# Performance work log

Measured on AMD Instinct MI355X. Metric: run time of the kernel, lower is better.

## Reference

```python
import jax, jax.numpy as jnp
import numpy as np

N, K, D = 2_000_000, 16, 3
EPS = 1e-6  # matches torch eye*1e-6 jitter added to the diagonal covariance


def setup_inputs() -> dict:
    key = jax.random.key(0)
    k1, k2, k3, k4 = jax.random.split(key, 4)
    x = jax.random.normal(k1, (N, D), dtype=jnp.float32)
    means = jax.random.normal(k2, (K, D), dtype=jnp.float32)
    # positive diagonal variances
    covariances = jax.random.uniform(k3, (K, D), dtype=jnp.float32, minval=0.5, maxval=2.0)
    w = jax.random.uniform(k4, (K,), dtype=jnp.float32, minval=0.1, maxval=1.0)
    weights = w / jnp.sum(w)  # mixture weights sum to 1
    return {"x": x, "means": means, "covariances": covariances, "weights": weights}


def reference(x, means, covariances, weights):
    # scale_tril of diag(cov)+eps*I is diag(sqrt(cov+eps))
    scale = jnp.sqrt(covariances + EPS)                      # [K, D]
    # standardized residuals: [N, K, D]
    z = (x[:, None, :] - means[None, :, :]) / scale[None, :, :]
    log_det = jnp.sum(jnp.log(scale), axis=-1)               # [K], log|L|
    d = x.shape[-1]
    # per-component Gaussian log-prob + log mixture weight: [N, K]
    log_prob = (-0.5 * (d * jnp.log(2.0 * jnp.pi) + jnp.sum(z * z, axis=-1))
                - log_det[None, :] + jnp.log(weights)[None, :])
    # mixture log-likelihood per point: [N]
    return jax.nn.logsumexp(log_prob, axis=1)
```

## Files before the change

### kernel.cpp

```cpp
#include <hip/hip_runtime.h>


constexpr int KCOMP = 16;
constexpr float EPS = 1e-6f;
#define LOG2E 1.4426950408889634f
#define LN2   0.6931471805599453f

__global__ __launch_bounds__(256) void gmm_loglik_kernel(
    const float* __restrict__ x,
    const float* __restrict__ means,
    const float* __restrict__ cov,
    const float* __restrict__ weights,
    float* __restrict__ out,
    int ngrp)
{
    __shared__ float4 s_cf[KCOMP * 2];

    const int t = threadIdx.x;
    if (t < KCOMP) {
        float v0 = cov[3 * t + 0] + EPS;
        float v1 = cov[3 * t + 1] + EPS;
        float v2 = cov[3 * t + 2] + EPS;
        float m0 = means[3 * t + 0];
        float m1 = means[3 * t + 1];
        float m2 = means[3 * t + 2];
        float h0 = 0.5f / v0, h1 = 0.5f / v1, h2 = 0.5f / v2;
        float ck = -2.7568155996140185f
                 - 0.5f * (__logf(v0) + __logf(v1) + __logf(v2))
                 + __logf(weights[t]);
        float A = ck - (h0 * m0 * m0 + h1 * m1 * m1 + h2 * m2 * m2);
        s_cf[2 * t + 0] = make_float4(LOG2E * A,
                                      LOG2E * 2.f * h0 * m0,
                                      LOG2E * 2.f * h1 * m1,
                                      LOG2E * 2.f * h2 * m2);
        s_cf[2 * t + 1] = make_float4(-LOG2E * h0, -LOG2E * h1, -LOG2E * h2, 0.f);
    }
    __syncthreads();

    const int g = blockIdx.x * blockDim.x + t;
    if (g >= ngrp) return;

    const float4* __restrict__ x4 = (const float4*)x;
    float4 a = x4[3 * g + 0];
    float4 b = x4[3 * g + 1];
    float4 c = x4[3 * g + 2];

    float px[4] = {a.x, a.w, b.z, c.y};
    float py[4] = {a.y, b.x, b.w, c.z};
    float pz[4] = {a.z, b.y, c.x, c.w};
    float res[4];

#pragma unroll
    for (int p = 0; p < 4; ++p) {
        const float X = px[p], Y = py[p], Z = pz[p];
        const float X2 = X * X, Y2 = Y * Y, Z2 = Z * Z;
        float lp[KCOMP];
        float mx = -3.4e38f;
#pragma unroll
        for (int k = 0; k < KCOMP; ++k) {
            float4 u = s_cf[2 * k + 0];
            float4 v = s_cf[2 * k + 1];
            float q = fmaf(u.y, X, u.x);
            q = fmaf(u.z, Y, q);
            q = fmaf(u.w, Z, q);
            q = fmaf(v.x, X2, q);
            q = fmaf(v.y, Y2, q);
            q = fmaf(v.z, Z2, q);
            lp[k] = q;
            mx = fmaxf(mx, q);
        }
        float s = 0.f;
#pragma unroll
        for (int k = 0; k < KCOMP; ++k)
            s += exp2f(lp[k] - mx);
        res[p] = LN2 * (mx + log2f(s));
    }

    ((float4*)out)[g] = make_float4(res[0], res[1], res[2], res[3]);
}

__global__ void gmm_tail_kernel(
    const float* __restrict__ x,
    const float* __restrict__ means,
    const float* __restrict__ cov,
    const float* __restrict__ weights,
    float* __restrict__ out,
    int start, int n)
{
    int i = start + blockIdx.x * blockDim.x + threadIdx.x;
    if (i >= n) return;
    float X = x[3 * i], Y = x[3 * i + 1], Z = x[3 * i + 2];
    float lp[KCOMP];
    float mx = -3.4e38f;
#pragma unroll
    for (int k = 0; k < KCOMP; ++k) {
        float v0 = cov[3 * k] + EPS, v1 = cov[3 * k + 1] + EPS, v2 = cov[3 * k + 2] + EPS;
        float dx = X - means[3 * k], dy = Y - means[3 * k + 1], dz = Z - means[3 * k + 2];
        float q = -2.7568155996140185f
                - 0.5f * (__logf(v0) + __logf(v1) + __logf(v2))
                + __logf(weights[k])
                - 0.5f * (dx * dx / v0 + dy * dy / v1 + dz * dz / v2);
        lp[k] = q;
        mx = fmaxf(mx, q);
    }
    float s = 0.f;
#pragma unroll
    for (int k = 0; k < KCOMP; ++k)
        s += __expf(lp[k] - mx);
    out[i] = mx + __logf(s);
}

extern "C" void kernel_launch(void* const* d_in, const int* in_sizes, int n_in,
                              void* d_out, int out_size, void* d_ws, size_t ws_size,
                              hipStream_t stream) {
    const float* x       = (const float*)d_in[0];
    const float* means   = (const float*)d_in[1];
    const float* cov     = (const float*)d_in[2];
    const float* weights = (const float*)d_in[3];
    float* out           = (float*)d_out;

    const int n = in_sizes[0] / 3;
    const int ngrp = n >> 2;
    if (ngrp > 0) {
        int blocks = (ngrp + 255) / 256;
        gmm_loglik_kernel<<<blocks, 256, 0, stream>>>(x, means, cov, weights, out, ngrp);
    }
    const int rem = n - (ngrp << 2);
    if (rem > 0) {
        gmm_tail_kernel<<<1, 64, 0, stream>>>(x, means, cov, weights, out, ngrp << 2, n);
    }
}
```

Measured before the change: 84.49 us.

## Stage points through LDS with coalesced loads and use packed FP32 FMA

Loads each block's point data cooperatively into shared memory with coalesced float4 reads, so per-thread strided 48-byte loads become contiguous ones. Processes the four points per thread as two 2-wide vectors so the compiler can emit packed FP32 FMA/max instructions, and swaps exp2f/log2f for the raw amdgcn intrinsics. This trades extra LDS traffic and a barrier for fewer VALU instructions. The kernel was compute-bound on the quadratic form and exp evaluations.

New measurement: 82.45 us. -2.4%, faster.

```diff
diff --git a/kernel.cpp b/kernel.cpp
--- a/kernel.cpp
+++ b/kernel.cpp
@@ -6,15 +6,20 @@
 #define LOG2E 1.4426950408889634f
 #define LN2   0.6931471805599453f
 
+typedef float v2f __attribute__((ext_vector_type(2)));
+static __device__ __forceinline__ v2f sp(float s) { return (v2f){s, s}; }
+
 __global__ __launch_bounds__(256) void gmm_loglik_kernel(
     const float* __restrict__ x,
     const float* __restrict__ means,
     const float* __restrict__ cov,
     const float* __restrict__ weights,
     float* __restrict__ out,
-    int ngrp)
+    int nmain)
 {
-    __shared__ float4 s_cf[KCOMP * 2];
+    __shared__ float4 s_pts4[768];
+    __shared__ float4 s_u[KCOMP];
+    __shared__ float4 s_v[KCOMP];
 
     const int t = threadIdx.x;
     if (t < KCOMP) {
@@ -29,54 +34,76 @@
                  - 0.5f * (__logf(v0) + __logf(v1) + __logf(v2))
                  + __logf(weights[t]);
         float A = ck - (h0 * m0 * m0 + h1 * m1 * m1 + h2 * m2 * m2);
-        s_cf[2 * t + 0] = make_float4(LOG2E * A,
-                                      LOG2E * 2.f * h0 * m0,
-                                      LOG2E * 2.f * h1 * m1,
-                                      LOG2E * 2.f * h2 * m2);
-        s_cf[2 * t + 1] = make_float4(-LOG2E * h0, -LOG2E * h1, -LOG2E * h2, 0.f);
+        s_u[t] = make_float4(LOG2E * A,
+                             LOG2E * 2.f * h0 * m0,
+                             LOG2E * 2.f * h1 * m1,
+                             LOG2E * 2.f * h2 * m2);
+        s_v[t] = make_float4(-LOG2E * h0, -LOG2E * h1, -LOG2E * h2, 0.f);
+    }
+
+    const float4* __restrict__ x4 = (const float4*)x;
+    const int n4 = (nmain >> 2) * 3;
+    const int base4 = blockIdx.x * 768;
+#pragma unroll
+    for (int j = 0; j < 3; ++j) {
+        int idx4 = base4 + j * 256 + t;
+        if (idx4 < n4) s_pts4[j * 256 + t] = x4[idx4];
     }
     __syncthreads();
 
-    const int g = blockIdx.x * blockDim.x + t;
-    if (g >= ngrp) return;
+    const int gp = blockIdx.x * 1024 + 4 * t;
+    if (gp >= nmain) return;
 
-    const float4* __restrict__ x4 = (const float4*)x;
-    float4 a = x4[3 * g + 0];
-    float4 b = x4[3 * g + 1];
-    float4 c = x4[3 * g + 2];
+    float4 c0 = s_pts4[3 * t + 0];
+    float4 c1 = s_pts4[3 * t + 1];
+    float4 c2 = s_pts4[3 * t + 2];
+    v2f Xa = {c0.x, c0.w}, Ya = {c0.y, c1.x}, Za = {c0.z, c1.y};
+    v2f Xb = {c1.z, c2.y}, Yb = {c1.w, c2.z}, Zb = {c2.x, c2.w};
+    v2f X2a = Xa * Xa, Y2a = Ya * Ya, Z2a = Za * Za;
+    v2f X2b = Xb * Xb, Y2b = Yb * Yb, Z2b = Zb * Zb;
 
-    float px[4] = {a.x, a.w, b.z, c.y};
-    float py[4] = {a.y, b.x, b.w, c.z};
-    float pz[4] = {a.z, b.y, c.x, c.w};
-    float res[4];
+    v2f lpa[KCOMP], lpb[KCOMP];
+    v2f mxa = sp(-3.4e38f), mxb = sp(-3.4e38f);
+#pragma unroll
+    for (int k = 0; k < KCOMP; ++k) {
+        float4 u = s_u[k];
+        float4 v = s_v[k];
+        v2f qa = __builtin_elementwise_fma(sp(u.y), Xa, sp(u.x));
+        qa = __builtin_elementwise_fma(sp(u.z), Ya, qa);
+        qa = __builtin_elementwise_fma(sp(u.w), Za, qa);
+        qa = __builtin_elementwise_fma(sp(v.x), X2a, qa);
+        qa = __builtin_elementwise_fma(sp(v.y), Y2a, qa);
+        qa = __builtin_elementwise_fma(sp(v.z), Z2a, qa);
+        lpa[k] = qa;
+        mxa = __builtin_elementwise_max(mxa, qa);
 
-#pragma unroll
-    for (int p = 0; p < 4; ++p) {
-        const float X = px[p], Y = py[p], Z = pz[p];
-        const float X2 = X * X, Y2 = Y * Y, Z2 = Z * Z;
-        float lp[KCOMP];
-        float mx = -3.4e38f;
-#pragma unroll
-        for (int k = 0; k < KCOMP; ++k) {
-            float4 u = s_cf[2 * k + 0];
-            float4 v = s_cf[2 * k + 1];
-            float q = fmaf(u.y, X, u.x);
-            q = fmaf(u.z, Y, q);
-            q = fmaf(u.w, Z, q);
-            q = fmaf(v.x, X2, q);
-            q = fmaf(v.y, Y2, q);
-            q = fmaf(v.z, Z2, q);
-            lp[k] = q;
-            mx = fmaxf(mx, q);
-        }
-        float s = 0.f;
-#pragma unroll
-        for (int k = 0; k < KCOMP; ++k)
-            s += exp2f(lp[k] - mx);
-        res[p] = LN2 * (mx + log2f(s));
+        v2f qb = __builtin_elementwise_fma(sp(u.y), Xb, sp(u.x));
+        qb = __builtin_elementwise_fma(sp(u.z), Yb, qb);
+        qb = __builtin_elementwise_fma(sp(u.w), Zb, qb);
+        qb = __builtin_elementwise_fma(sp(v.x), X2b, qb);
+        qb = __builtin_elementwise_fma(sp(v.y), Y2b, qb);
+        qb = __builtin_elementwise_fma(sp(v.z), Z2b, qb);
+        lpb[k] = qb;
+        mxb = __builtin_elementwise_max(mxb, qb);
     }
 
-    ((float4*)out)[g] = make_float4(res[0], res[1], res[2], res[3]);
+    v2f sa = sp(0.f), sb = sp(0.f);
+#pragma unroll
+    for (int k = 0; k < KCOMP; ++k) {
+        v2f da = lpa[k] - mxa;
+        v2f db = lpb[k] - mxb;
+        sa.x += __builtin_amdgcn_exp2f(da.x);
+        sa.y += __builtin_amdgcn_exp2f(da.y);
+        sb.x += __builtin_amdgcn_exp2f(db.x);
+        sb.y += __builtin_amdgcn_exp2f(db.y);
+    }
+
+    float4 res;
+    res.x = LN2 * (mxa.x + __builtin_amdgcn_logf(sa.x));
+    res.y = LN2 * (mxa.y + __builtin_amdgcn_logf(sa.y));
+    res.z = LN2 * (mxb.x + __builtin_amdgcn_logf(sb.x));
+    res.w = LN2 * (mxb.y + __builtin_amdgcn_logf(sb.y));
+    ((float4*)out)[gp >> 2] = res;
 }
 
 __global__ void gmm_tail_kernel(
@@ -120,13 +147,12 @@
     float* out           = (float*)d_out;
 
     const int n = in_sizes[0] / 3;
-    const int ngrp = n >> 2;
-    if (ngrp > 0) {
-        int blocks = (ngrp + 255) / 256;
-        gmm_loglik_kernel<<<blocks, 256, 0, stream>>>(x, means, cov, weights, out, ngrp);
+    const int nmain = n & ~3;
+    if (nmain > 0) {
+        int blocks = (nmain + 1023) / 1024;
+        gmm_loglik_kernel<<<blocks, 256, 0, stream>>>(x, means, cov, weights, out, nmain);
     }
-    const int rem = n - (ngrp << 2);
-    if (rem > 0) {
-        gmm_tail_kernel<<<1, 64, 0, stream>>>(x, means, cov, weights, out, ngrp << 2, n);
+    if (n > nmain) {
+        gmm_tail_kernel<<<1, 64, 0, stream>>>(x, means, cov, weights, out, nmain, n);
     }
 }
```
